# Optimization experiments

Measured on AMD Instinct MI355X. Metric: run time of the kernel, lower is better.

## Reference

```python
import jax, jax.numpy as jnp
import numpy as np

NP_, NC_, F_, H_ = 50000, 10000, 128, 256
E_ANN, E_LINK, E_PPI, NPAIR = 400000, 160000, 800000, 200000


def _edges(key, E, n_src, n_dst):
    # random edges with src != dst (PyG GATConv removes then re-adds self loops;
    # generating none keeps the edge set fixed under that transform)
    k1, k2 = jax.random.split(key)
    src = jax.random.randint(k1, (E,), 0, n_src)
    dst = (src + 1 + jax.random.randint(k2, (E,), 0, n_dst - 1)) % n_dst
    return jnp.stack([src, dst]).astype(jnp.int32)


def setup_inputs() -> dict:
    key = jax.random.key(0)
    ks = jax.random.split(key, 20)
    g = lambda k, shape, s: jax.random.normal(k, shape, dtype=jnp.float32) * s
    sF, sH = 1.0 / np.sqrt(F_), 1.0 / np.sqrt(H_)
    inp = {}
    inp['xp'] = g(ks[0], (NP_, F_), 1.0)
    inp['xc'] = g(ks[1], (NC_, F_), 1.0)
    inp['ei_pann'] = _edges(ks[2], E_ANN, NP_, NC_)
    inp['ei_nann'] = _edges(ks[3], E_ANN, NP_, NC_)
    inp['ei_link'] = _edges(ks[4], E_LINK, NC_, NC_)
    inp['ei_ppi'] = _edges(ks[5], E_PPI, NP_, NP_)
    inp['mask'] = jax.random.randint(ks[6], (NPAIR, 2), 0, NP_).astype(jnp.int32)
    # GAT params, stacked over edge types [0]=+annotation, [1]=-annotation, [2]=ppi
    inp['Wa'] = g(ks[7], (3, F_, H_), sF)
    inp['att_src_a'] = g(ks[8], (3, H_), sH)
    inp['att_dst_a'] = g(ks[9], (3, H_), sH)
    inp['bias_a'] = jnp.zeros((3, H_), jnp.float32)
    inp['Wb'] = g(ks[10], (3, H_, F_), sH)
    inp['att_src_b'] = g(ks[11], (3, F_), sF)
    inp['att_dst_b'] = g(ks[12], (3, F_), sF)
    inp['bias_b'] = jnp.zeros((3, F_), jnp.float32)
    # GraphConv (class->class) params
    inp['Wrel_a'] = g(ks[13], (F_, H_), sF)
    inp['Wroot_a'] = g(ks[14], (F_, H_), sF)
    inp['brel_a'] = jnp.zeros((H_,), jnp.float32)
    inp['Wrel_b'] = g(ks[15], (H_, F_), sH)
    inp['Wroot_b'] = g(ks[16], (H_, F_), sH)
    inp['brel_b'] = jnp.zeros((F_,), jnp.float32)
    inp['W_out'] = g(ks[17], (2 * F_, 1), 1.0 / np.sqrt(2 * F_))
    inp['b_out'] = jnp.zeros((1,), jnp.float32)
    return inp


def _gat(x_src, x_dst, ei, W, a_s, a_d, b):
    # PyG GATConv, heads=1, negative_slope=0.2, add_self_loops=True (num_nodes=min)
    n_src, n_dst = x_src.shape[0], x_dst.shape[0]
    loops = jnp.arange(min(n_src, n_dst), dtype=ei.dtype)
    src = jnp.concatenate([ei[0], loops])
    dst = jnp.concatenate([ei[1], loops])
    hs = x_src @ W                                     # [N_src, out]
    hd = x_dst @ W                                     # [N_dst, out]
    e = jax.nn.leaky_relu((hs @ a_s)[src] + (hd @ a_d)[dst], 0.2)  # [E]
    m = jax.ops.segment_max(e, dst, num_segments=n_dst)
    ex = jnp.exp(e - m[dst])
    denom = jax.ops.segment_sum(ex, dst, num_segments=n_dst)
    alpha = ex / denom[dst]                            # segment softmax over dst
    out = jax.ops.segment_sum(alpha[:, None] * hs[src], dst, num_segments=n_dst)
    return out + b


def _graph_conv(x, ei, W_rel, W_root, b_rel):
    # PyG GraphConv, aggr='add': lin_rel(sum_j x_j) + lin_root(x_i)
    agg = jax.ops.segment_sum(x[ei[0]], ei[1], num_segments=x.shape[0])
    return agg @ W_rel + b_rel + x @ W_root


def reference(xp, xc, ei_pann, ei_nann, ei_link, ei_ppi, mask,
              Wa, att_src_a, att_dst_a, bias_a,
              Wb, att_src_b, att_dst_b, bias_b,
              Wrel_a, Wroot_a, brel_a, Wrel_b, Wroot_b, brel_b,
              W_out, b_out):
    # ---- HeteroConv layer a (sum-aggregate over edge types per dst type) ----
    hc = (_gat(xp, xc, ei_pann, Wa[0], att_src_a[0], att_dst_a[0], bias_a[0])
          + _gat(xp, xc, ei_nann, Wa[1], att_src_a[1], att_dst_a[1], bias_a[1])
          + _graph_conv(xc, ei_link, Wrel_a, Wroot_a, brel_a))
    hp = _gat(xp, xp, ei_ppi, Wa[2], att_src_a[2], att_dst_a[2], bias_a[2])
    hc = jax.nn.relu(hc)  # dropout p=0.0 -> identity
    hp = jax.nn.relu(hp)
    # ---- HeteroConv layer b ----
    hc2 = (_gat(hp, hc, ei_pann, Wb[0], att_src_b[0], att_dst_b[0], bias_b[0])
           + _gat(hp, hc, ei_nann, Wb[1], att_src_b[1], att_dst_b[1], bias_b[1])
           + _graph_conv(hc, ei_link, Wrel_b, Wroot_b, brel_b))
    del hc2  # class embeddings are computed but unused by the original forward
    hp2 = _gat(hp, hp, ei_ppi, Wb[2], att_src_b[2], att_dst_b[2], bias_b[2])
    # ---- link prediction head ----
    mT = mask.T
    p1 = jax.lax.stop_gradient(hp2[mT[0]])  # .detach() in the original
    p2 = jax.lax.stop_gradient(hp2[mT[1]])
    h = jnp.concatenate([p1, p2], axis=1)   # [n_pairs, 2*F]
    return jax.nn.sigmoid(h @ W_out + b_out)
```

## Files before the change

kernel.cpp:

```cpp
#include <hip/hip_runtime.h>
#include <hip/hip_bf16.h>
#include <math.h>

#define NP 50000
#define F 128
#define H 256
#define E_PPI 800000
#define ET (E_PPI + NP)
#define NPAIR 200000
#define CAP 96
#define FILL_BLOCKS ((ET + 255) / 256)

typedef __attribute__((ext_vector_type(8))) short short8v;
typedef __attribute__((ext_vector_type(4))) float float4v;
typedef __attribute__((ext_vector_type(2))) float float2v;
typedef __attribute__((ext_vector_type(4))) unsigned int uint4v;

__device__ __forceinline__ short f2bs(float f) {
  unsigned u = __builtin_bit_cast(unsigned, f);
  unsigned r = (u + 0x7FFFu + ((u >> 16) & 1u)) >> 16;
  return (short)r;
}
__device__ __forceinline__ float bs2f(short s) {
  unsigned u = ((unsigned)(unsigned short)s) << 16;
  return __builtin_bit_cast(float, u);
}
__device__ __forceinline__ float lrelu(float t) { return (t > 0.f) ? t : 0.2f * t; }

__device__ __forceinline__ float2v bf2x2(unsigned d) {
  float2v f;
  f.x = __builtin_bit_cast(float, d << 16);
  f.y = __builtin_bit_cast(float, d & 0xFFFF0000u);
  return f;
}
__device__ __forceinline__ float2v pkfma(float2v a, float2v b, float2v c) {
#if __has_builtin(__builtin_elementwise_fma)
  return __builtin_elementwise_fma(a, b, c);
#else
  float2v r; r.x = fmaf(a.x, b.x, c.x); r.y = fmaf(a.y, b.y, c.y); return r;
#endif
}


template<int K, int N>
__device__ __forceinline__ void pack_one(const float* __restrict__ B, short* __restrict__ Bp,
                                         int idx) {
  constexpr int KB = K / 32;
  int lane = idx & 63;
  int rest = idx >> 6;
  int kb = rest % KB;
  int tile = rest / KB;
  int n = tile * 16 + (lane & 15);
  int k0 = kb * 32 + (lane >> 4) * 8;
  size_t base = (size_t)idx * 8;
#pragma unroll
  for (int j = 0; j < 8; ++j) Bp[base + j] = f2bs(B[(size_t)(k0 + j) * N + n]);
}

__global__ void fill_pack(const int* __restrict__ src_idx, const int* __restrict__ dst_idx,
                          int* __restrict__ deg, int* __restrict__ bucket,
                          const float* __restrict__ Wa, const float* __restrict__ Wb,
                          short* __restrict__ BaP, short* __restrict__ BbP,
                          const float* __restrict__ bb, const float* __restrict__ Wout,
                          float* __restrict__ consts) {
  int b = blockIdx.x;
  if (b < FILL_BLOCKS) {
    int k = b * 256 + threadIdx.x;
    if (k >= ET) return;
    int s, d;
    if (k < E_PPI) { s = src_idx[k]; d = dst_idx[k]; }
    else           { s = d = k - E_PPI; }
    int pos = atomicAdd(&deg[d], 1);
    if (pos < CAP) bucket[(size_t)d * CAP + pos] = s;
  } else if (b < FILL_BLOCKS + 32) {
    int idx = (b - FILL_BLOCKS) * 256 + threadIdx.x;
    if (idx < 4096)      pack_one<F, H>(Wa, BaP, idx);
    else                 pack_one<H, F>(Wb, BbP, idx - 4096);
  } else {
    int lane = threadIdx.x;
    if (lane >= 64) return;
    float b0 = bb[lane], b1 = bb[lane + 64];
    float c1 = fmaf(b0, Wout[lane], b1 * Wout[lane + 64]);
    float c2 = fmaf(b0, Wout[128 + lane], b1 * Wout[192 + lane]);
#pragma unroll
    for (int o = 32; o; o >>= 1) {
      c1 += __shfl_xor(c1, o);
      c2 += __shfl_xor(c2, o);
    }
    if (lane == 0) { consts[0] = c1; consts[1] = c2; }
  }
}


template<int K, int N, bool AF32, bool HEAD>
__launch_bounds__(256)
__global__ void gemm_mfma(const void* __restrict__ Av, const short* __restrict__ Bp,
                          short* __restrict__ Cb, const float* __restrict__ a_s,
                          const float* __restrict__ a_d, const float* __restrict__ W1,
                          const float* __restrict__ W2, float* __restrict__ sb,
                          float* __restrict__ db, float2v* __restrict__ pq) {
  constexpr int KB = K / 32;
  constexpr int TPW = N / 64;
  __shared__ float sred[4][16];
  __shared__ float dred[4][16];
  __shared__ float pred[4][16];
  __shared__ float qred[4][16];
  int lane = threadIdx.x & 63, wave = threadIdx.x >> 6;
  int ln16 = lane & 15, quad = lane >> 4;
  int m0 = blockIdx.x * 16;
  float4v acc[TPW];
#pragma unroll
  for (int t = 0; t < TPW; ++t) acc[t] = (float4v)0.f;
#pragma unroll
  for (int kb = 0; kb < KB; ++kb) {
    int ka = kb * 32 + quad * 8;
    short8v ah;
    if constexpr (AF32) {
      const float* ap = (const float*)Av + (size_t)(m0 + ln16) * K + ka;
      float4v a0 = *(const float4v*)ap;
      float4v a1 = *(const float4v*)(ap + 4);
#pragma unroll
      for (int j = 0; j < 4; ++j) { ah[j] = f2bs(a0[j]); ah[4 + j] = f2bs(a1[j]); }
    } else {
      ah = *(const short8v*)((const short*)Av + (size_t)(m0 + ln16) * K + ka);
    }
#pragma unroll
    for (int t = 0; t < TPW; ++t) {
      int tile = wave * TPW + t;
      short8v bh = *(const short8v*)(Bp + ((size_t)(tile * KB + kb) * 64 + lane) * 8);
      acc[t] = __builtin_amdgcn_mfma_f32_16x16x32_bf16(ah, bh, acc[t], 0, 0, 0);
    }
  }
  if constexpr (!HEAD) {
#pragma unroll
    for (int t = 0; t < TPW; ++t) {
      int cc = (wave * TPW + t) * 16 + ln16;
#pragma unroll
      for (int r = 0; r < 4; ++r) {
        int rr = m0 + quad * 4 + r;
        Cb[(size_t)rr * N + cc] = f2bs(acc[t][r]);
      }
    }
  }
  float su[4] = {0.f, 0.f, 0.f, 0.f}, dv[4] = {0.f, 0.f, 0.f, 0.f};
  float pu[4] = {0.f, 0.f, 0.f, 0.f}, qv[4] = {0.f, 0.f, 0.f, 0.f};
#pragma unroll
  for (int t = 0; t < TPW; ++t) {
    int cc = (wave * TPW + t) * 16 + ln16;
    float as = a_s[cc], ad = a_d[cc];
    float w1 = HEAD ? W1[cc] : 0.f, w2 = HEAD ? W2[cc] : 0.f;
#pragma unroll
    for (int r = 0; r < 4; ++r) {
      su[r] = fmaf(acc[t][r], as, su[r]);
      dv[r] = fmaf(acc[t][r], ad, dv[r]);
      if constexpr (HEAD) {
        pu[r] = fmaf(acc[t][r], w1, pu[r]);
        qv[r] = fmaf(acc[t][r], w2, qv[r]);
      }
    }
  }
#pragma unroll
  for (int r = 0; r < 4; ++r) {
    for (int off = 1; off < 16; off <<= 1) {
      su[r] += __shfl_xor(su[r], off);
      dv[r] += __shfl_xor(dv[r], off);
      if constexpr (HEAD) {
        pu[r] += __shfl_xor(pu[r], off);
        qv[r] += __shfl_xor(qv[r], off);
      }
    }
  }
  if (ln16 == 0) {
#pragma unroll
    for (int r = 0; r < 4; ++r) {
      sred[wave][quad * 4 + r] = su[r];
      dred[wave][quad * 4 + r] = dv[r];
      if constexpr (HEAD) {
        pred[wave][quad * 4 + r] = pu[r];
        qred[wave][quad * 4 + r] = qv[r];
      }
    }
  }
  __syncthreads();
  if (threadIdx.x < 16) {
    int row = threadIdx.x;
    sb[m0 + row] = sred[0][row] + sred[1][row] + sred[2][row] + sred[3][row];
    db[m0 + row] = dred[0][row] + dred[1][row] + dred[2][row] + dred[3][row];
    if constexpr (HEAD) {
      float2v t;
      t.x = pred[0][row] + pred[1][row] + pred[2][row] + pred[3][row];
      t.y = qred[0][row] + qred[1][row] + qred[2][row] + qred[3][row];
      pq[m0 + row] = t;
    }
  }
}


__launch_bounds__(256)
__global__ void agg_a(const short* __restrict__ h, const int* __restrict__ bucket,
                      const int* __restrict__ degv, const float* __restrict__ sb,
                      const float* __restrict__ db, const float* __restrict__ bias,
                      short* __restrict__ outb) {
  int gid = blockIdx.x * blockDim.x + threadIdx.x;
  int dst = gid >> 6, lane = gid & 63;
  if (dst >= NP) return;
  int half = lane >> 5, l32 = lane & 31;
  const int* row = bucket + (size_t)dst * CAP;
  int deg = degv[dst];
  float di = db[dst];
  float m = -1e30f, ssum = 0.f, x0 = -1e30f;
  for (int c0 = 0; c0 < deg; c0 += 64) {
    int idx = c0 + lane;
    float x = -1e30f;
    if (idx < deg) x = lrelu(sb[row[idx]] + di);
    if (c0 == 0) x0 = x;
    float cm = x;
#pragma unroll
    for (int o = 32; o; o >>= 1) cm = fmaxf(cm, __shfl_xor(cm, o));
    float nm = fmaxf(m, cm);
    float ex = (idx < deg) ? __expf(x - nm) : 0.f;
#pragma unroll
    for (int o = 32; o; o >>= 1) ex += __shfl_xor(ex, o);
    ssum = ssum * __expf(m - nm) + ex;
    m = nm;
  }
  float inv = 1.0f / ssum;
  float w0 = __expf(x0 - m);
  float2v acc2[4];
#pragma unroll
  for (int k = 0; k < 4; ++k) acc2[k] = (float2v)0.f;
  for (int it0 = 0; it0 < deg; it0 += 4) {
    int e1 = it0 + half, e2 = it0 + 2 + half;
    bool v1 = (e1 < deg), v2 = (e2 < deg);
    int s1 = v1 ? row[e1] : row[0];
    int s2 = v2 ? row[e2] : row[0];
    short8v xa = *(const short8v*)(h + (size_t)s1 * 256 + l32 * 8);
    short8v xb = *(const short8v*)(h + (size_t)s2 * 256 + l32 * 8);
    float w1 = __shfl(w0, e1 & 63);
    float w2 = __shfl(w0, e2 & 63);
    if (deg > 64) {
      if (e1 >= 64 && v1) w1 = __expf(lrelu(sb[s1] + di) - m);
      if (e2 >= 64 && v2) w2 = __expf(lrelu(sb[s2] + di) - m);
    }
    w1 = v1 ? w1 : 0.f;
    w2 = v2 ? w2 : 0.f;
    uint4v da = __builtin_bit_cast(uint4v, xa);
    uint4v dbv = __builtin_bit_cast(uint4v, xb);
    float2v W1 = {w1, w1}, W2 = {w2, w2};
#pragma unroll
    for (int k = 0; k < 4; ++k) {
      acc2[k] = pkfma(bf2x2(da[k]), W1, acc2[k]);
      acc2[k] = pkfma(bf2x2(dbv[k]), W2, acc2[k]);
    }
  }
#pragma unroll
  for (int k = 0; k < 4; ++k) {
    acc2[k].x += __shfl_xor(acc2[k].x, 32);
    acc2[k].y += __shfl_xor(acc2[k].y, 32);
  }
  if (half == 0) {
    short8v o;
#pragma unroll
    for (int k = 0; k < 4; ++k) {
      o[2 * k]     = f2bs(fmaxf(fmaf(acc2[k].x, inv, bias[l32 * 8 + 2 * k]),     0.f));
      o[2 * k + 1] = f2bs(fmaxf(fmaf(acc2[k].y, inv, bias[l32 * 8 + 2 * k + 1]), 0.f));
    }
    *(short8v*)(outb + (size_t)dst * 256 + l32 * 8) = o;
  }
}


__launch_bounds__(256)
__global__ void agg_uv(const int* __restrict__ bucket, const int* __restrict__ degv,
                       const float* __restrict__ sb, const float* __restrict__ db,
                       const float2v* __restrict__ pq, float* __restrict__ u,
                       float* __restrict__ v_out) {
  int gid = blockIdx.x * blockDim.x + threadIdx.x;
  int dst = gid >> 6, lane = gid & 63;
  if (dst >= NP) return;
  const int* row = bucket + (size_t)dst * CAP;
  int deg = degv[dst];
  float di = db[dst];
  float m = -1e30f, ssum = 0.f, uacc = 0.f, vacc = 0.f;
  for (int c0 = 0; c0 < deg; c0 += 64) {
    int idx = c0 + lane;
    bool val = idx < deg;
    int src = val ? row[idx] : row[0];
    float x = val ? lrelu(sb[src] + di) : -1e30f;
    float2v pqv = pq[src];
    float cm = x;
#pragma unroll
    for (int o = 32; o; o >>= 1) cm = fmaxf(cm, __shfl_xor(cm, o));
    float nm = fmaxf(m, cm);
    float scale = __expf(m - nm);
    float ex = val ? __expf(x - nm) : 0.f;
    float eu = ex * pqv.x, ev = ex * pqv.y;
#pragma unroll
    for (int o = 32; o; o >>= 1) {
      ex += __shfl_xor(ex, o);
      eu += __shfl_xor(eu, o);
      ev += __shfl_xor(ev, o);
    }
    ssum = ssum * scale + ex;
    uacc = uacc * scale + eu;
    vacc = vacc * scale + ev;
    m = nm;
  }
  if (lane == 0) {
    float inv = 1.0f / ssum;
    u[dst] = uacc * inv;
    v_out[dst] = vacc * inv;
  }
}


__global__ void out_kernel(const int* __restrict__ mask, const float* __restrict__ u,
                           const float* __restrict__ v, const float* __restrict__ bout,
                           const float* __restrict__ consts, float* __restrict__ out) {
  int p = blockIdx.x * blockDim.x + threadIdx.x;
  if (p >= NPAIR) return;
  int a = mask[2 * p], b = mask[2 * p + 1];
  float logit = u[a] + v[b] + bout[0] + consts[0] + consts[1];
  out[p] = 1.0f / (1.0f + __expf(-logit));
}


extern "C" void kernel_launch(void* const* d_in, const int* in_sizes, int n_in,
                              void* d_out, int out_size, void* d_ws, size_t ws_size,
                              hipStream_t stream) {
  const float* xp   = (const float*)d_in[0];
  const int*   ei   = (const int*)d_in[5];
  const int*   mask = (const int*)d_in[6];
  const float* Wa2  = (const float*)d_in[7]  + 2 * F * H;
  const float* asa  = (const float*)d_in[8]  + 2 * H;
  const float* ada  = (const float*)d_in[9]  + 2 * H;
  const float* ba   = (const float*)d_in[10] + 2 * H;
  const float* Wb2  = (const float*)d_in[11] + 2 * H * F;
  const float* asb  = (const float*)d_in[12] + 2 * F;
  const float* adb  = (const float*)d_in[13] + 2 * F;
  const float* bb   = (const float*)d_in[14] + 2 * F;
  const float* Wout = (const float*)d_in[21];
  const float* bout = (const float*)d_in[22];
  float* out = (float*)d_out;

  char* ws = (char*)d_ws;
  size_t off = 0;
  auto alloc = [&](size_t bytes) {
    void* p = ws + off;
    off = (off + bytes + 255) & ~(size_t)255;
    return p;
  };
  short* h1b     = (short*)alloc((size_t)NP * H * 2);
  short* hpb     = (short*)alloc((size_t)NP * H * 2);
  int*   bucket  = (int*)alloc((size_t)NP * CAP * 4);
  int*   deg     = (int*)alloc((size_t)NP * 4);
  float* sb      = (float*)alloc((size_t)NP * 4);
  float* db      = (float*)alloc((size_t)NP * 4);
  float2v* pq    = (float2v*)alloc((size_t)NP * 8);
  float* u       = (float*)alloc((size_t)NP * 4);
  float* v       = (float*)alloc((size_t)NP * 4);
  short* BaP     = (short*)alloc((size_t)F * H * 2);
  short* BbP     = (short*)alloc((size_t)H * F * 2);
  float* consts  = (float*)alloc(2 * 4);

  const int* src_idx = ei;
  const int* dst_idx = ei + E_PPI;

  hipMemsetAsync(deg, 0, (size_t)NP * 4, stream);
  fill_pack<<<FILL_BLOCKS + 33, 256, 0, stream>>>(src_idx, dst_idx, deg, bucket,
                                                  Wa2, Wb2, BaP, BbP, bb, Wout, consts);

  int node_wave_blocks = NP / 4;

  gemm_mfma<F, H, true, false><<<NP / 16, 256, 0, stream>>>(
      xp, BaP, h1b, asa, ada, nullptr, nullptr, sb, db, nullptr);
  agg_a<<<node_wave_blocks, 256, 0, stream>>>(h1b, bucket, deg, sb, db, ba, hpb);

  gemm_mfma<H, F, false, true><<<NP / 16, 256, 0, stream>>>(
      hpb, BbP, nullptr, asb, adb, Wout, Wout + F, sb, db, pq);
  agg_uv<<<node_wave_blocks, 256, 0, stream>>>(bucket, deg, sb, db, pq, u, v);

  out_kernel<<<(NPAIR + 255) / 256, 256, 0, stream>>>(mask, u, v, bout, consts, out);
}
```

Before: 300.0 us.

## Fold second-layer weight into attention and head vectors, drop second GEMM

Layer b's outputs are only used through dot products with att_src, att_dst and the two W_out halves. This change precomputes Wb times each of those four vectors and has the layer-a aggregation kernel emit the four scalars per node directly. That removes the hp bf16 buffer write and read and the whole second MFMA GEMM launch. In exchange the aggregation epilogue does a per-node 256-wide reduction against four vectors, and rounding changes because hp is no longer quantized to bf16.

After: 284.6 us. 1.05x faster.

```diff
diff --git a/kernel.cpp b/kernel.cpp
--- a/kernel.cpp
+++ b/kernel.cpp
@@ -59,10 +59,11 @@
 
 __global__ void fill_pack(const int* __restrict__ src_idx, const int* __restrict__ dst_idx,
                           int* __restrict__ deg, int* __restrict__ bucket,
-                          const float* __restrict__ Wa, const float* __restrict__ Wb,
-                          short* __restrict__ BaP, short* __restrict__ BbP,
-                          const float* __restrict__ bb, const float* __restrict__ Wout,
-                          float* __restrict__ consts) {
+                          const float* __restrict__ Wa, short* __restrict__ BaP,
+                          const float* __restrict__ Wb, const float* __restrict__ asb,
+                          const float* __restrict__ adb, const float* __restrict__ Wout,
+                          float* __restrict__ wvec,
+                          const float* __restrict__ bb, float* __restrict__ consts) {
   int b = blockIdx.x;
   if (b < FILL_BLOCKS) {
     int k = b * 256 + threadIdx.x;
@@ -72,10 +73,19 @@
     else           { s = d = k - E_PPI; }
     int pos = atomicAdd(&deg[d], 1);
     if (pos < CAP) bucket[(size_t)d * CAP + pos] = s;
-  } else if (b < FILL_BLOCKS + 32) {
+  } else if (b < FILL_BLOCKS + 16) {
     int idx = (b - FILL_BLOCKS) * 256 + threadIdx.x;
-    if (idx < 4096)      pack_one<F, H>(Wa, BaP, idx);
-    else                 pack_one<H, F>(Wb, BbP, idx - 4096);
+    pack_one<F, H>(Wa, BaP, idx);
+  } else if (b < FILL_BLOCKS + 20) {
+    int t = (b - FILL_BLOCKS - 16) * 256 + threadIdx.x;
+    int vec = t >> 8, k = t & 255;
+    const float* srcv = (vec == 0) ? asb : (vec == 1) ? adb
+                      : (vec == 2) ? Wout : (Wout + F);
+    const float* wrow = Wb + (size_t)k * F;
+    float acc = 0.f;
+#pragma unroll 4
+    for (int j = 0; j < F; ++j) acc = fmaf(wrow[j], srcv[j], acc);
+    wvec[vec * 256 + k] = acc;
   } else {
     int lane = threadIdx.x;
     if (lane >= 64) return;
@@ -92,19 +102,16 @@
 }
 
 
-template<int K, int N, bool AF32, bool HEAD>
 __launch_bounds__(256)
-__global__ void gemm_mfma(const void* __restrict__ Av, const short* __restrict__ Bp,
-                          short* __restrict__ Cb, const float* __restrict__ a_s,
-                          const float* __restrict__ a_d, const float* __restrict__ W1,
-                          const float* __restrict__ W2, float* __restrict__ sb,
-                          float* __restrict__ db, float2v* __restrict__ pq) {
+__global__ void gemm_a(const float* __restrict__ A, const short* __restrict__ Bp,
+                       short* __restrict__ Cb, const float* __restrict__ a_s,
+                       const float* __restrict__ a_d, float* __restrict__ sb,
+                       float* __restrict__ db) {
+  constexpr int K = F, N = H;
   constexpr int KB = K / 32;
   constexpr int TPW = N / 64;
   __shared__ float sred[4][16];
   __shared__ float dred[4][16];
-  __shared__ float pred[4][16];
-  __shared__ float qred[4][16];
   int lane = threadIdx.x & 63, wave = threadIdx.x >> 6;
   int ln16 = lane & 15, quad = lane >> 4;
   int m0 = blockIdx.x * 16;
@@ -114,16 +121,12 @@
 #pragma unroll
   for (int kb = 0; kb < KB; ++kb) {
     int ka = kb * 32 + quad * 8;
+    const float* ap = A + (size_t)(m0 + ln16) * K + ka;
+    float4v a0 = *(const float4v*)ap;
+    float4v a1 = *(const float4v*)(ap + 4);
     short8v ah;
-    if constexpr (AF32) {
-      const float* ap = (const float*)Av + (size_t)(m0 + ln16) * K + ka;
-      float4v a0 = *(const float4v*)ap;
-      float4v a1 = *(const float4v*)(ap + 4);
-#pragma unroll
-      for (int j = 0; j < 4; ++j) { ah[j] = f2bs(a0[j]); ah[4 + j] = f2bs(a1[j]); }
-    } else {
-      ah = *(const short8v*)((const short*)Av + (size_t)(m0 + ln16) * K + ka);
-    }
+#pragma unroll
+    for (int j = 0; j < 4; ++j) { ah[j] = f2bs(a0[j]); ah[4 + j] = f2bs(a1[j]); }
 #pragma unroll
     for (int t = 0; t < TPW; ++t) {
       int tile = wave * TPW + t;
@@ -131,32 +134,24 @@
       acc[t] = __builtin_amdgcn_mfma_f32_16x16x32_bf16(ah, bh, acc[t], 0, 0, 0);
     }
   }
-  if constexpr (!HEAD) {
-#pragma unroll
-    for (int t = 0; t < TPW; ++t) {
-      int cc = (wave * TPW + t) * 16 + ln16;
-#pragma unroll
-      for (int r = 0; r < 4; ++r) {
-        int rr = m0 + quad * 4 + r;
-        Cb[(size_t)rr * N + cc] = f2bs(acc[t][r]);
-      }
+#pragma unroll
+  for (int t = 0; t < TPW; ++t) {
+    int cc = (wave * TPW + t) * 16 + ln16;
+#pragma unroll
+    for (int r = 0; r < 4; ++r) {
+      int rr = m0 + quad * 4 + r;
+      Cb[(size_t)rr * N + cc] = f2bs(acc[t][r]);
     }
   }
   float su[4] = {0.f, 0.f, 0.f, 0.f}, dv[4] = {0.f, 0.f, 0.f, 0.f};
-  float pu[4] = {0.f, 0.f, 0.f, 0.f}, qv[4] = {0.f, 0.f, 0.f, 0.f};
 #pragma unroll
   for (int t = 0; t < TPW; ++t) {
     int cc = (wave * TPW + t) * 16 + ln16;
     float as = a_s[cc], ad = a_d[cc];
-    float w1 = HEAD ? W1[cc] : 0.f, w2 = HEAD ? W2[cc] : 0.f;
 #pragma unroll
     for (int r = 0; r < 4; ++r) {
       su[r] = fmaf(acc[t][r], as, su[r]);
       dv[r] = fmaf(acc[t][r], ad, dv[r]);
-      if constexpr (HEAD) {
-        pu[r] = fmaf(acc[t][r], w1, pu[r]);
-        qv[r] = fmaf(acc[t][r], w2, qv[r]);
-      }
     }
   }
 #pragma unroll
@@ -164,10 +159,6 @@
     for (int off = 1; off < 16; off <<= 1) {
       su[r] += __shfl_xor(su[r], off);
       dv[r] += __shfl_xor(dv[r], off);
-      if constexpr (HEAD) {
-        pu[r] += __shfl_xor(pu[r], off);
-        qv[r] += __shfl_xor(qv[r], off);
-      }
     }
   }
   if (ln16 == 0) {
@@ -175,10 +166,6 @@
     for (int r = 0; r < 4; ++r) {
       sred[wave][quad * 4 + r] = su[r];
       dred[wave][quad * 4 + r] = dv[r];
-      if constexpr (HEAD) {
-        pred[wave][quad * 4 + r] = pu[r];
-        qred[wave][quad * 4 + r] = qv[r];
-      }
     }
   }
   __syncthreads();
@@ -186,12 +173,6 @@
     int row = threadIdx.x;
     sb[m0 + row] = sred[0][row] + sred[1][row] + sred[2][row] + sred[3][row];
     db[m0 + row] = dred[0][row] + dred[1][row] + dred[2][row] + dred[3][row];
-    if constexpr (HEAD) {
-      float2v t;
-      t.x = pred[0][row] + pred[1][row] + pred[2][row] + pred[3][row];
-      t.y = qred[0][row] + qred[1][row] + qred[2][row] + qred[3][row];
-      pq[m0 + row] = t;
-    }
   }
 }
 
@@ -200,7 +181,9 @@
 __global__ void agg_a(const short* __restrict__ h, const int* __restrict__ bucket,
                       const int* __restrict__ degv, const float* __restrict__ sb,
                       const float* __restrict__ db, const float* __restrict__ bias,
-                      short* __restrict__ outb) {
+                      const float* __restrict__ wvec,
+                      float* __restrict__ sb2, float* __restrict__ db2,
+                      float2v* __restrict__ pq) {
   int gid = blockIdx.x * blockDim.x + threadIdx.x;
   int dst = gid >> 6, lane = gid & 63;
   if (dst >= NP) return;
@@ -258,14 +241,32 @@
     acc2[k].x += __shfl_xor(acc2[k].x, 32);
     acc2[k].y += __shfl_xor(acc2[k].y, 32);
   }
-  if (half == 0) {
-    short8v o;
-#pragma unroll
-    for (int k = 0; k < 4; ++k) {
-      o[2 * k]     = f2bs(fmaxf(fmaf(acc2[k].x, inv, bias[l32 * 8 + 2 * k]),     0.f));
-      o[2 * k + 1] = f2bs(fmaxf(fmaf(acc2[k].y, inv, bias[l32 * 8 + 2 * k + 1]), 0.f));
-    }
-    *(short8v*)(outb + (size_t)dst * 256 + l32 * 8) = o;
+  float ts = 0.f, td = 0.f, tp = 0.f, tq = 0.f;
+#pragma unroll
+  for (int k = 0; k < 4; ++k) {
+#pragma unroll
+    for (int half_c = 0; half_c < 2; ++half_c) {
+      int c = l32 * 8 + 2 * k + half_c;
+      float a = half_c ? acc2[k].y : acc2[k].x;
+      float o = fmaxf(fmaf(a, inv, bias[c]), 0.f);
+      ts = fmaf(o, wvec[c], ts);
+      td = fmaf(o, wvec[256 + c], td);
+      tp = fmaf(o, wvec[512 + c], tp);
+      tq = fmaf(o, wvec[768 + c], tq);
+    }
+  }
+#pragma unroll
+  for (int o = 1; o < 32; o <<= 1) {
+    ts += __shfl_xor(ts, o);
+    td += __shfl_xor(td, o);
+    tp += __shfl_xor(tp, o);
+    tq += __shfl_xor(tq, o);
+  }
+  if (lane == 0) {
+    sb2[dst] = ts;
+    db2[dst] = td;
+    float2v t; t.x = tp; t.y = tq;
+    pq[dst] = t;
   }
 }
 
@@ -351,34 +352,32 @@
     return p;
   };
   short* h1b     = (short*)alloc((size_t)NP * H * 2);
-  short* hpb     = (short*)alloc((size_t)NP * H * 2);
   int*   bucket  = (int*)alloc((size_t)NP * CAP * 4);
   int*   deg     = (int*)alloc((size_t)NP * 4);
   float* sb      = (float*)alloc((size_t)NP * 4);
   float* db      = (float*)alloc((size_t)NP * 4);
+  float* sb2     = (float*)alloc((size_t)NP * 4);
+  float* db2     = (float*)alloc((size_t)NP * 4);
   float2v* pq    = (float2v*)alloc((size_t)NP * 8);
   float* u       = (float*)alloc((size_t)NP * 4);
   float* v       = (float*)alloc((size_t)NP * 4);
   short* BaP     = (short*)alloc((size_t)F * H * 2);
-  short* BbP     = (short*)alloc((size_t)H * F * 2);
+  float* wvec    = (float*)alloc(4 * 256 * 4);
   float* consts  = (float*)alloc(2 * 4);
 
   const int* src_idx = ei;
   const int* dst_idx = ei + E_PPI;
 
   hipMemsetAsync(deg, 0, (size_t)NP * 4, stream);
-  fill_pack<<<FILL_BLOCKS + 33, 256, 0, stream>>>(src_idx, dst_idx, deg, bucket,
-                                                  Wa2, Wb2, BaP, BbP, bb, Wout, consts);
+  fill_pack<<<FILL_BLOCKS + 21, 256, 0, stream>>>(src_idx, dst_idx, deg, bucket,
+                                                  Wa2, BaP, Wb2, asb, adb, Wout,
+                                                  wvec, bb, consts);
 
   int node_wave_blocks = NP / 4;
 
-  gemm_mfma<F, H, true, false><<<NP / 16, 256, 0, stream>>>(
-      xp, BaP, h1b, asa, ada, nullptr, nullptr, sb, db, nullptr);
-  agg_a<<<node_wave_blocks, 256, 0, stream>>>(h1b, bucket, deg, sb, db, ba, hpb);
-
-  gemm_mfma<H, F, false, true><<<NP / 16, 256, 0, stream>>>(
-      hpb, BbP, nullptr, asb, adb, Wout, Wout + F, sb, db, pq);
-  agg_uv<<<node_wave_blocks, 256, 0, stream>>>(bucket, deg, sb, db, pq, u, v);
-
+  gemm_a<<<NP / 16, 256, 0, stream>>>(xp, BaP, h1b, asa, ada, sb, db);
+  agg_a<<<node_wave_blocks, 256, 0, stream>>>(h1b, bucket, deg, sb, db, ba,
+                                              wvec, sb2, db2, pq);
+  agg_uv<<<node_wave_blocks, 256, 0, stream>>>(bucket, deg, sb2, db2, pq, u, v);
   out_kernel<<<(NPAIR + 255) / 256, 256, 0, stream>>>(mask, u, v, bout, consts, out);
 }
```
